# Performance work log

Measured on AMD Instinct MI355X. Metric: run time of the kernel, lower is better.

## Reference

```python
import jax, jax.numpy as jnp
import numpy as np

EPS = 1e-5
CHUNK = 512


def _bn(x, gamma, beta):
    # BatchNorm1d in training mode: biased batch statistics over the batch dim
    m = x.mean(axis=0)
    v = ((x - m) ** 2).mean(axis=0)
    return (x - m) * jax.lax.rsqrt(v + EPS) * gamma + beta


def _xavier(k, fan_in, fan_out):
    lim = float(np.sqrt(6.0 / (fan_in + fan_out)))
    return jax.random.uniform(k, (fan_in, fan_out), minval=-lim, maxval=lim, dtype=jnp.float32)


def setup_inputs() -> dict:
    key = jax.random.key(0)
    ks = jax.random.split(key, 10)
    B, CH_S, CH_H, T = 8192, 512, 2048, 3
    D = CH_H * T  # 6144 = 12 chunks of 512
    inp = {
        "fs": jax.random.normal(ks[0], (B, CH_S), dtype=jnp.float32),
        "ft0": jax.random.normal(ks[1], (B, CH_H), dtype=jnp.float32),
        "ft1": jax.random.normal(ks[2], (B, CH_H), dtype=jnp.float32),
        "ft2": jax.random.normal(ks[3], (B, CH_H), dtype=jnp.float32),
        # fixed (non-trainable in the original: plain tensor) score key [512, 1]
        "score_key": jax.random.uniform(ks[4], (CHUNK, 1), dtype=jnp.float32),
        # align_t: Linear(D,2048) -> BN -> Linear(2048,2048) -> BN -> Linear(2048,CH_H) -> ReLU
        "W1": _xavier(ks[5], D, 2048), "b1": jnp.zeros((2048,), jnp.float32),
        "g1": jnp.ones((2048,), jnp.float32), "beta1": jnp.zeros((2048,), jnp.float32),
        "W2": _xavier(ks[6], 2048, 2048), "b2": jnp.zeros((2048,), jnp.float32),
        "g2": jnp.ones((2048,), jnp.float32), "beta2": jnp.zeros((2048,), jnp.float32),
        "W3": _xavier(ks[7], 2048, CH_H), "b3": jnp.zeros((CH_H,), jnp.float32),
        # extend: Linear(CH_H, D) -> ReLU
        "We": _xavier(ks[8], CH_H, D), "bE": jnp.zeros((D,), jnp.float32),
    }
    return inp


def reference(fs, ft0, ft1, ft2, score_key, W1, b1, g1, beta1, W2, b2, g2, beta2, W3, b3, We, bE):
    # fs is accepted but unused, mirroring the original forward
    ft_all = jnp.concatenate([ft0, ft1, ft2], axis=1)  # [B, D]
    B, D = ft_all.shape
    n_chunks = D // CHUNK
    chunks = ft_all.reshape(B, n_chunks, CHUNK)  # [B, C, 512]
    # chunked score matmul against key[512,1], softmax over chunks
    score = jax.nn.softmax(jnp.einsum("bck,k->bc", chunks, score_key[:, 0]), axis=1)  # [B, C]
    # per-chunk reweighting: x <- x + x*score  == x*(1+score), one broadcasted multiply
    ft_all = (chunks * (1.0 + score[:, :, None])).reshape(B, D)
    # align_t MLP (BatchNorm in training mode, no activation between first layers)
    h = _bn(ft_all @ W1 + b1, g1, beta1)
    h = _bn(h @ W2 + b2, g2, beta2)
    aligned_t = jax.nn.relu(h @ W3 + b3)
    extend_t = jax.nn.relu(aligned_t @ We + bE)
    return aligned_t, extend_t, ft_all
```

## Files before the change

### kernel.cpp

```cpp
#include <hip/hip_runtime.h>
#include <hip/hip_bf16.h>
#include <cstdint>
#include <cstddef>

using bf16x8 = __attribute__((ext_vector_type(8))) __bf16;
using f32x4  = __attribute__((ext_vector_type(4))) float;

__device__ __forceinline__ unsigned short f2bf(float f) {
  unsigned int u = __float_as_uint(f);
  u += 0x7FFFu + ((u >> 16) & 1u);
  return (unsigned short)(u >> 16);
}

__device__ __forceinline__ void async_cp16(const void* g, void* l) {
  __builtin_amdgcn_global_load_lds(
      (const __attribute__((address_space(1))) unsigned int*)g,
      (__attribute__((address_space(3))) unsigned int*)l, 16, 0, 0);
}

__global__ __launch_bounds__(256) void wconv(const float* __restrict__ W,
                                             unsigned short* __restrict__ Wt,
                                             int K, int N) {
  __shared__ float tile[32][33];
  const int n0 = blockIdx.x * 32;
  const int k0 = blockIdx.y * 32;
  const int tx = threadIdx.x;
  const int ty = threadIdx.y;
  for (int i = 0; i < 32; i += 8)
    tile[ty + i][tx] = W[(size_t)(k0 + ty + i) * N + n0 + tx];
  __syncthreads();
  for (int i = 0; i < 32; i += 8)
    Wt[(size_t)(n0 + ty + i) * K + k0 + tx] = f2bf(tile[tx][ty + i]);
}

__global__ __launch_bounds__(256) void score_kernel(
    const float* __restrict__ ft0, const float* __restrict__ ft1,
    const float* __restrict__ ft2, const float* __restrict__ key,
    float* __restrict__ out_f, unsigned short* __restrict__ out_b) {
  const int row  = blockIdx.x;
  const int t    = threadIdx.x;
  const int lane = t & 63;
  const int w    = t >> 6;
  const int h    = t >> 7;
  __shared__ float wsum[6][4];
  __shared__ float mult[12];

  const float4* k4 = (const float4*)key;
  float4 v[6];
#pragma unroll
  for (int i = 0; i < 6; i++) {
    const int idx4 = t + 256 * i;
    const int e    = idx4 * 4;
    const float* tsrc = (i < 2) ? ft0 : (i < 4) ? ft1 : ft2;
    v[i] = *(const float4*)(tsrc + (size_t)row * 2048 + (e & 2047));
    float4 kv = k4[idx4 & 127];
    float p = v[i].x * kv.x + v[i].y * kv.y + v[i].z * kv.z + v[i].w * kv.w;
#pragma unroll
    for (int o = 32; o > 0; o >>= 1) p += __shfl_down(p, o, 64);
    if (lane == 0) wsum[i][w] = p;
  }
  __syncthreads();
  if (t == 0) {
    float s[12];
    float mx = -1e30f;
    for (int c = 0; c < 12; c++) {
      s[c] = wsum[c >> 1][2 * (c & 1)] + wsum[c >> 1][2 * (c & 1) + 1];
      mx = fmaxf(mx, s[c]);
    }
    float tot = 0.f;
    for (int c = 0; c < 12; c++) { s[c] = expf(s[c] - mx); tot += s[c]; }
    const float inv = 1.0f / tot;
    for (int c = 0; c < 12; c++) mult[c] = 1.0f + s[c] * inv;
  }
  __syncthreads();
#pragma unroll
  for (int i = 0; i < 6; i++) {
    const int idx4 = t + 256 * i;
    const int e    = idx4 * 4;
    const float m  = mult[2 * i + h];
    float4 o;
    o.x = v[i].x * m; o.y = v[i].y * m; o.z = v[i].z * m; o.w = v[i].w * m;
    *(float4*)(out_f + (size_t)row * 6144 + e) = o;
    ushort4 ob;
    ob.x = f2bf(o.x); ob.y = f2bf(o.y); ob.z = f2bf(o.z); ob.w = f2bf(o.w);
    *(ushort4*)(out_b + (size_t)row * 6144 + e) = ob;
  }
}

template <int EPI>
__global__ __launch_bounds__(512, 2) void gemm256(
    const unsigned short* __restrict__ A,
    const unsigned short* __restrict__ Bt,
    const float* __restrict__ bias,
    float* __restrict__ C,
    unsigned short* __restrict__ Cbf,
    float* __restrict__ ps,
    float* __restrict__ pq,
    int M, int N, int K) {
  __shared__ __align__(16) unsigned short smem[65536];
  __shared__ float bnred[8][4][16][2];
  const int t    = threadIdx.x;
  const int lane = t & 63;
  const int w    = t >> 6;
  const int wm   = w >> 2;
  const int wn   = w & 3;
  const int frow = lane & 15;
  const int quad = lane >> 4;

  const int NXg  = gridDim.x, NYg = gridDim.y;
  const int blin = blockIdx.x + NXg * blockIdx.y;
  const int rxcd = blin & 7;
  const int ib   = blin >> 3;
  const int RX   = NXg >> 1;
  const int RY   = NYg >> 2;
  const int bx   = (rxcd & 1) * RX + ib % RX;
  const int by   = (rxcd >> 1) * RY + ib / RX;
  const size_t m0 = (size_t)by * 256;
  const size_t n0 = (size_t)bx * 256;

  const bool isB  = w >= 4;
  const int  seg  = (w & 3) * 4096;
  const int  off0 = seg + lane * 16;
  const int  pos0 = off0 ^ (((off0 >> 7) & 7) << 4);
  const int  r0   = pos0 >> 6;
  const int  kb0  = pos0 & 63;
  const unsigned short* gp =
      (isB ? Bt + (n0 + (size_t)r0) * K : A + (m0 + (size_t)r0) * K) + (kb0 >> 1);
  char* lseg = (char*)smem + (isB ? 16384 : 0) + seg;

  const int offA = (wm * 128 + frow) * 64 + quad * 16;
  const int aoff = offA ^ (((offA >> 7) & 7) << 4);
  const int offB = (wn * 64 + frow) * 64 + quad * 16;
  const int boff = 16384 + (offB ^ (((offB >> 7) & 7) << 4));

  f32x4 acc[8][4];
  const f32x4 z = {0.f, 0.f, 0.f, 0.f};
#pragma unroll
  for (int i = 0; i < 8; i++)
#pragma unroll
    for (int j = 0; j < 4; j++) acc[i][j] = z;

  const int nkt = K >> 5;

  auto stage = [&](int slot) {
    char* lb = lseg + slot * 32768;
    async_cp16(gp,                  lb);
    async_cp16(gp + (size_t)16 * K, lb + 1024);
    async_cp16(gp + (size_t)32 * K, lb + 2048);
    async_cp16(gp + (size_t)48 * K, lb + 3072);
    gp += 32;
  };

  auto ldfrag = [&](int slot, bf16x8* fa, bf16x8* fb) {
    const char* base = (const char*)smem + slot * 32768;
#pragma unroll
    for (int mi = 0; mi < 8; ++mi)
      fa[mi] = *(const bf16x8*)(base + aoff + mi * 1024);
#pragma unroll
    for (int ni = 0; ni < 4; ++ni)
      fb[ni] = *(const bf16x8*)(base + boff + ni * 1024);
  };

  auto domfma = [&](const bf16x8* fa, const bf16x8* fb) {
    __builtin_amdgcn_s_setprio(1);
#pragma unroll
    for (int mi = 0; mi < 8; ++mi)
#pragma unroll
      for (int ni = 0; ni < 4; ++ni)
        acc[mi][ni] = __builtin_amdgcn_mfma_f32_16x16x32_bf16(fa[mi], fb[ni], acc[mi][ni], 0, 0, 0);
    __builtin_amdgcn_s_setprio(0);
  };

  bf16x8 fa0[8], fb0[4], fa1[8], fb1[4];

  stage(0); stage(1); stage(2);
  asm volatile("s_waitcnt vmcnt(4)\n\ts_barrier" ::: "memory");
  ldfrag(0, fa0, fb0);

  int kt = 0;
  for (; kt + 4 < nkt; kt += 2) {
    stage((kt + 3) & 3);
    domfma(fa0, fb0);
    ldfrag((kt + 1) & 3, fa1, fb1);
    asm volatile("s_waitcnt vmcnt(4)\n\ts_barrier" ::: "memory");
    stage((kt + 4) & 3);
    domfma(fa1, fb1);
    ldfrag((kt + 2) & 3, fa0, fb0);
    asm volatile("s_waitcnt vmcnt(4)\n\ts_barrier" ::: "memory");
  }
  stage((nkt - 1) & 3);
  domfma(fa0, fb0);
  ldfrag((nkt - 3) & 3, fa1, fb1);
  asm volatile("s_waitcnt vmcnt(4)\n\ts_barrier" ::: "memory");
  domfma(fa1, fb1);
  ldfrag((nkt - 2) & 3, fa0, fb0);
  asm volatile("s_waitcnt vmcnt(0)\n\ts_barrier" ::: "memory");
  domfma(fa0, fb0);
  ldfrag((nkt - 1) & 3, fa1, fb1);
  domfma(fa1, fb1);

  float s4[4] = {0.f, 0.f, 0.f, 0.f};
  float q4[4] = {0.f, 0.f, 0.f, 0.f};
#pragma unroll
  for (int mi = 0; mi < 8; ++mi) {
    const size_t rowb = m0 + wm * 128 + mi * 16 + quad * 4;
#pragma unroll
    for (int ni = 0; ni < 4; ++ni) {
      const size_t col = n0 + wn * 64 + ni * 16 + frow;
      const float bvs = bias[col];
#pragma unroll
      for (int r = 0; r < 4; ++r) {
        float v = acc[mi][ni][r] + bvs;
        if (EPI == 1) v = fmaxf(v, 0.f);
        const size_t idx = (rowb + r) * (size_t)N + col;
        C[idx] = v;
        if (EPI == 1 && Cbf != nullptr) Cbf[idx] = f2bf(v);
        if (EPI == 0) { s4[ni] += v; q4[ni] += v * v; }
      }
    }
  }
  if (EPI == 0) {
#pragma unroll
    for (int ni = 0; ni < 4; ++ni) {
      s4[ni] += __shfl_down(s4[ni], 16, 64);
      s4[ni] += __shfl_down(s4[ni], 32, 64);
      q4[ni] += __shfl_down(q4[ni], 16, 64);
      q4[ni] += __shfl_down(q4[ni], 32, 64);
    }
    if (quad == 0) {
#pragma unroll
      for (int ni = 0; ni < 4; ++ni) {
        bnred[w][ni][frow][0] = s4[ni];
        bnred[w][ni][frow][1] = q4[ni];
      }
    }
    __syncthreads();
    if (w < 4 && quad == 0) {
#pragma unroll
      for (int ni = 0; ni < 4; ++ni) {
        const size_t col = n0 + (size_t)w * 64 + ni * 16 + frow;
        const float ss = bnred[w][ni][frow][0] + bnred[w + 4][ni][frow][0];
        const float qq = bnred[w][ni][frow][1] + bnred[w + 4][ni][frow][1];
        ps[(size_t)by * N + col] = ss;
        pq[(size_t)by * N + col] = qq;
      }
    }
  }
}

__global__ __launch_bounds__(256) void bn_final(const float* __restrict__ ps,
                                                const float* __restrict__ pq,
                                                const float* __restrict__ g,
                                                const float* __restrict__ beta,
                                                float* __restrict__ stats,
                                                int N, int nb, float invM) {
  const int c = blockIdx.x * 256 + threadIdx.x;
  float s = 0.f, q = 0.f;
  for (int b = 0; b < nb; b++) { s += ps[(size_t)b * N + c]; q += pq[(size_t)b * N + c]; }
  const float mean = s * invM;
  const float var  = q * invM - mean * mean;
  const float sc   = g[c] * rsqrtf(var + 1e-5f);
  stats[c]     = sc;
  stats[N + c] = beta[c] - mean * sc;
}

__global__ __launch_bounds__(256) void bn_norm(const float* __restrict__ h,
                                               const float* __restrict__ stats,
                                               unsigned short* __restrict__ hb, int N) {
  const size_t i4 = (size_t)blockIdx.x * 256 + threadIdx.x;
  const float4 x = ((const float4*)h)[i4];
  const int c = (int)((i4 * 4) & (size_t)(N - 1));
  const float4 sc = *(const float4*)(stats + c);
  const float4 tt = *(const float4*)(stats + N + c);
  ushort4 ob;
  ob.x = f2bf(x.x * sc.x + tt.x);
  ob.y = f2bf(x.y * sc.y + tt.y);
  ob.z = f2bf(x.z * sc.z + tt.z);
  ob.w = f2bf(x.w * sc.w + tt.w);
  ((ushort4*)hb)[i4] = ob;
}

extern "C" void kernel_launch(void* const* d_in, const int* in_sizes, int n_in,
                              void* d_out, int out_size, void* d_ws, size_t ws_size,
                              hipStream_t stream) {
  const float* ft0 = (const float*)d_in[1];
  const float* ft1 = (const float*)d_in[2];
  const float* ft2 = (const float*)d_in[3];
  const float* key = (const float*)d_in[4];
  const float* W1  = (const float*)d_in[5];
  const float* b1  = (const float*)d_in[6];
  const float* g1  = (const float*)d_in[7];
  const float* be1 = (const float*)d_in[8];
  const float* W2  = (const float*)d_in[9];
  const float* b2  = (const float*)d_in[10];
  const float* g2  = (const float*)d_in[11];
  const float* be2 = (const float*)d_in[12];
  const float* W3  = (const float*)d_in[13];
  const float* b3  = (const float*)d_in[14];
  const float* We  = (const float*)d_in[15];
  const float* bE  = (const float*)d_in[16];

  float* out         = (float*)d_out;
  float* out_aligned = out;
  float* out_extend  = out + (size_t)8192 * 2048;
  float* out_ft      = out + (size_t)8192 * 2048 + (size_t)8192 * 6144;

  char* ws = (char*)d_ws;
  unsigned short* ft_bf = (unsigned short*)(ws);
  unsigned short* Wt1   = (unsigned short*)(ws + 100663296ull);
  unsigned short* Wt2   = (unsigned short*)(ws + 125829120ull);
  unsigned short* Wt3   = (unsigned short*)(ws + 134217728ull);
  unsigned short* WtE   = (unsigned short*)(ws + 142606336ull);
  float*          hf    = (float*)(ws + 167772160ull);
  unsigned short* hba   = (unsigned short*)(ws + 234881024ull);
  unsigned short* hbb   = (unsigned short*)(ws + 268435456ull);
  float*          psum  = (float*)(ws + 301989888ull);
  float*          psq   = (float*)(ws + 302252032ull);
  float*          stats = (float*)(ws + 302514176ull);

  const dim3 blk32(32, 8);
  wconv<<<dim3(2048 / 32, 6144 / 32), blk32, 0, stream>>>(W1, Wt1, 6144, 2048);
  wconv<<<dim3(2048 / 32, 2048 / 32), blk32, 0, stream>>>(W2, Wt2, 2048, 2048);
  wconv<<<dim3(2048 / 32, 2048 / 32), blk32, 0, stream>>>(W3, Wt3, 2048, 2048);
  wconv<<<dim3(6144 / 32, 2048 / 32), blk32, 0, stream>>>(We, WtE, 2048, 6144);

  score_kernel<<<dim3(8192), dim3(256), 0, stream>>>(ft0, ft1, ft2, key, out_ft, ft_bf);

  gemm256<0><<<dim3(8, 32), dim3(512), 0, stream>>>(ft_bf, Wt1, b1, hf,
                                                    (unsigned short*)nullptr, psum, psq,
                                                    8192, 2048, 6144);
  bn_final<<<dim3(8), dim3(256), 0, stream>>>(psum, psq, g1, be1, stats, 2048, 32, 1.0f / 8192.0f);
  bn_norm<<<dim3(16384), dim3(256), 0, stream>>>(hf, stats, hba, 2048);

  gemm256<0><<<dim3(8, 32), dim3(512), 0, stream>>>(hba, Wt2, b2, hf,
                                                    (unsigned short*)nullptr, psum, psq,
                                                    8192, 2048, 2048);
  bn_final<<<dim3(8), dim3(256), 0, stream>>>(psum, psq, g2, be2, stats, 2048, 32, 1.0f / 8192.0f);
  bn_norm<<<dim3(16384), dim3(256), 0, stream>>>(hf, stats, hba, 2048);

  gemm256<1><<<dim3(8, 32), dim3(512), 0, stream>>>(hba, Wt3, b3, out_aligned, hbb,
                                                    (float*)nullptr, (float*)nullptr,
                                                    8192, 2048, 2048);
  gemm256<1><<<dim3(24, 32), dim3(512), 0, stream>>>(hbb, WtE, bE, out_extend,
                                                     (unsigned short*)nullptr,
                                                     (float*)nullptr, (float*)nullptr,
                                                     8192, 6144, 2048);
}
```

Before: 1.345 ms.

## Fold BatchNorm into next layer weights and switch GEMM to 32x32 MFMA

The BatchNorm scale and shift are folded into the following linear layer. Its weights are scaled per input row during the bf16 transpose, and the shift is turned into an adjusted bias through a small matrix-vector product. This removes the separate fp32 hidden write and the bn_norm pass: GEMMs now write pre-BN activations in bf16 directly. The GEMM also moves from 16x16x32 to 32x32x16 MFMA tiles and drops the XCD-aware block remapping. In exchange, BN statistics are computed from values later rounded to bf16, and the weight scaling adds rounding error when variances are small.

```diff
diff --git a/kernel.cpp b/kernel.cpp
--- a/kernel.cpp
+++ b/kernel.cpp
@@ -5,6 +5,7 @@
 
 using bf16x8 = __attribute__((ext_vector_type(8))) __bf16;
 using f32x4  = __attribute__((ext_vector_type(4))) float;
+using f32x16 = __attribute__((ext_vector_type(16))) float;
 
 __device__ __forceinline__ unsigned short f2bf(float f) {
   unsigned int u = __float_as_uint(f);
@@ -33,6 +34,41 @@
     Wt[(size_t)(n0 + ty + i) * K + k0 + tx] = f2bf(tile[tx][ty + i]);
 }
 
+__global__ __launch_bounds__(256) void wscale_t(const float* __restrict__ W,
+                                                const float* __restrict__ sc,
+                                                unsigned short* __restrict__ Wt,
+                                                int K, int N) {
+  __shared__ float tile[32][33];
+  const int n0 = blockIdx.x * 32;
+  const int k0 = blockIdx.y * 32;
+  const int tx = threadIdx.x;
+  const int ty = threadIdx.y;
+  for (int i = 0; i < 32; i += 8)
+    tile[ty + i][tx] = W[(size_t)(k0 + ty + i) * N + n0 + tx] * sc[k0 + ty + i];
+  __syncthreads();
+  for (int i = 0; i < 32; i += 8)
+    Wt[(size_t)(n0 + ty + i) * K + k0 + tx] = f2bf(tile[tx][ty + i]);
+}
+
+__global__ __launch_bounds__(256) void bvec_p(const float* __restrict__ W,
+                                              const float* __restrict__ tt,
+                                              float* __restrict__ pb, int N) {
+  const int c  = blockIdx.x * 256 + threadIdx.x;
+  const int k0 = blockIdx.y * 256;
+  float s = 0.f;
+  for (int k = 0; k < 256; ++k) s += tt[k0 + k] * W[(size_t)(k0 + k) * N + c];
+  pb[(size_t)blockIdx.y * N + c] = s;
+}
+
+__global__ __launch_bounds__(256) void bvec_f(const float* __restrict__ pb,
+                                              const float* __restrict__ b,
+                                              float* __restrict__ bs, int N, int nb) {
+  const int c = blockIdx.x * 256 + threadIdx.x;
+  float s = b[c];
+  for (int j = 0; j < nb; ++j) s += pb[(size_t)j * N + c];
+  bs[c] = s;
+}
+
 __global__ __launch_bounds__(256) void score_kernel(
     const float* __restrict__ ft0, const float* __restrict__ ft1,
     const float* __restrict__ ft2, const float* __restrict__ key,
@@ -98,23 +134,14 @@
     float* __restrict__ pq,
     int M, int N, int K) {
   __shared__ __align__(16) unsigned short smem[65536];
-  __shared__ float bnred[8][4][16][2];
+  __shared__ float bnred[8][2][32][2];
   const int t    = threadIdx.x;
   const int lane = t & 63;
   const int w    = t >> 6;
   const int wm   = w >> 2;
   const int wn   = w & 3;
-  const int frow = lane & 15;
-  const int quad = lane >> 4;
-
-  const int NXg  = gridDim.x, NYg = gridDim.y;
-  const int blin = blockIdx.x + NXg * blockIdx.y;
-  const int rxcd = blin & 7;
-  const int ib   = blin >> 3;
-  const int RX   = NXg >> 1;
-  const int RY   = NYg >> 2;
-  const int bx   = (rxcd & 1) * RX + ib % RX;
-  const int by   = (rxcd >> 1) * RY + ib / RX;
+  const int bx   = blockIdx.x;
+  const int by   = blockIdx.y;
   const size_t m0 = (size_t)by * 256;
   const size_t n0 = (size_t)bx * 256;
 
@@ -128,17 +155,19 @@
       (isB ? Bt + (n0 + (size_t)r0) * K : A + (m0 + (size_t)r0) * K) + (kb0 >> 1);
   char* lseg = (char*)smem + (isB ? 16384 : 0) + seg;
 
-  const int offA = (wm * 128 + frow) * 64 + quad * 16;
-  const int aoff = offA ^ (((offA >> 7) & 7) << 4);
-  const int offB = (wn * 64 + frow) * 64 + quad * 16;
-  const int boff = 16384 + (offB ^ (((offB >> 7) & 7) << 4));
-
-  f32x4 acc[8][4];
-  const f32x4 z = {0.f, 0.f, 0.f, 0.f};
-#pragma unroll
-  for (int i = 0; i < 8; i++)
-#pragma unroll
-    for (int j = 0; j < 4; j++) acc[i][j] = z;
+  const int r5  = lane & 31;
+  const int q16 = lane >> 5;
+  const int swz = ((r5 >> 1) & 7) << 4;
+  const int aBase = (((wm * 128 + r5) * 64 + q16 * 16) ^ swz);
+  const int bBase = 16384 + (((wn * 64 + r5) * 64 + q16 * 16) ^ swz);
+
+  f32x16 acc[4][2];
+#pragma unroll
+  for (int i = 0; i < 4; i++)
+#pragma unroll
+    for (int j = 0; j < 2; j++)
+#pragma unroll
+      for (int g = 0; g < 16; g++) acc[i][j][g] = 0.f;
 
   const int nkt = K >> 5;
 
@@ -154,20 +183,27 @@
   auto ldfrag = [&](int slot, bf16x8* fa, bf16x8* fb) {
     const char* base = (const char*)smem + slot * 32768;
 #pragma unroll
-    for (int mi = 0; mi < 8; ++mi)
-      fa[mi] = *(const bf16x8*)(base + aoff + mi * 1024);
-#pragma unroll
-    for (int ni = 0; ni < 4; ++ni)
-      fb[ni] = *(const bf16x8*)(base + boff + ni * 1024);
+    for (int mi = 0; mi < 4; ++mi) {
+      fa[mi * 2 + 0] = *(const bf16x8*)(base + (aBase       ) + mi * 2048);
+      fa[mi * 2 + 1] = *(const bf16x8*)(base + (aBase ^ 32  ) + mi * 2048);
+    }
+#pragma unroll
+    for (int ni = 0; ni < 2; ++ni) {
+      fb[ni * 2 + 0] = *(const bf16x8*)(base + (bBase       ) + ni * 2048);
+      fb[ni * 2 + 1] = *(const bf16x8*)(base + (bBase ^ 32  ) + ni * 2048);
+    }
   };
 
   auto domfma = [&](const bf16x8* fa, const bf16x8* fb) {
     __builtin_amdgcn_s_setprio(1);
 #pragma unroll
-    for (int mi = 0; mi < 8; ++mi)
-#pragma unroll
-      for (int ni = 0; ni < 4; ++ni)
-        acc[mi][ni] = __builtin_amdgcn_mfma_f32_16x16x32_bf16(fa[mi], fb[ni], acc[mi][ni], 0, 0, 0);
+    for (int kh = 0; kh < 2; ++kh)
+#pragma unroll
+      for (int mi = 0; mi < 4; ++mi)
+#pragma unroll
+        for (int ni = 0; ni < 2; ++ni)
+          acc[mi][ni] = __builtin_amdgcn_mfma_f32_32x32x16_bf16(
+              fa[mi * 2 + kh], fb[ni * 2 + kh], acc[mi][ni], 0, 0, 0);
     __builtin_amdgcn_s_setprio(0);
   };
 
@@ -199,50 +235,62 @@
   ldfrag((nkt - 1) & 3, fa1, fb1);
   domfma(fa1, fb1);
 
-  float s4[4] = {0.f, 0.f, 0.f, 0.f};
-  float q4[4] = {0.f, 0.f, 0.f, 0.f};
-#pragma unroll
-  for (int mi = 0; mi < 8; ++mi) {
-    const size_t rowb = m0 + wm * 128 + mi * 16 + quad * 4;
-#pragma unroll
-    for (int ni = 0; ni < 4; ++ni) {
-      const size_t col = n0 + wn * 64 + ni * 16 + frow;
+  const int cl = r5;
+  const int rh = q16 * 4;
+  if (EPI == 0) {
+    float s2[2] = {0.f, 0.f}, q2[2] = {0.f, 0.f};
+#pragma unroll
+    for (int ni = 0; ni < 2; ++ni) {
+      const size_t col = n0 + wn * 64 + ni * 32 + cl;
       const float bvs = bias[col];
 #pragma unroll
-      for (int r = 0; r < 4; ++r) {
-        float v = acc[mi][ni][r] + bvs;
-        if (EPI == 1) v = fmaxf(v, 0.f);
-        const size_t idx = (rowb + r) * (size_t)N + col;
-        C[idx] = v;
-        if (EPI == 1 && Cbf != nullptr) Cbf[idx] = f2bf(v);
-        if (EPI == 0) { s4[ni] += v; q4[ni] += v * v; }
+      for (int mi = 0; mi < 4; ++mi) {
+        const size_t rowb = m0 + wm * 128 + mi * 32 + rh;
+#pragma unroll
+        for (int g = 0; g < 16; ++g) {
+          float v = acc[mi][ni][g] + bvs;
+          const size_t row = rowb + (g & 3) + 8 * (g >> 2);
+          Cbf[row * (size_t)N + col] = f2bf(v);
+          s2[ni] += v; q2[ni] += v * v;
+        }
       }
     }
-  }
-  if (EPI == 0) {
-#pragma unroll
-    for (int ni = 0; ni < 4; ++ni) {
-      s4[ni] += __shfl_down(s4[ni], 16, 64);
-      s4[ni] += __shfl_down(s4[ni], 32, 64);
-      q4[ni] += __shfl_down(q4[ni], 16, 64);
-      q4[ni] += __shfl_down(q4[ni], 32, 64);
-    }
-    if (quad == 0) {
-#pragma unroll
-      for (int ni = 0; ni < 4; ++ni) {
-        bnred[w][ni][frow][0] = s4[ni];
-        bnred[w][ni][frow][1] = q4[ni];
+#pragma unroll
+    for (int ni = 0; ni < 2; ++ni) {
+      s2[ni] += __shfl_down(s2[ni], 32, 64);
+      q2[ni] += __shfl_down(q2[ni], 32, 64);
+    }
+    if (lane < 32) {
+#pragma unroll
+      for (int ni = 0; ni < 2; ++ni) {
+        bnred[w][ni][cl][0] = s2[ni];
+        bnred[w][ni][cl][1] = q2[ni];
       }
     }
     __syncthreads();
-    if (w < 4 && quad == 0) {
-#pragma unroll
-      for (int ni = 0; ni < 4; ++ni) {
-        const size_t col = n0 + (size_t)w * 64 + ni * 16 + frow;
-        const float ss = bnred[w][ni][frow][0] + bnred[w + 4][ni][frow][0];
-        const float qq = bnred[w][ni][frow][1] + bnred[w + 4][ni][frow][1];
-        ps[(size_t)by * N + col] = ss;
-        pq[(size_t)by * N + col] = qq;
+    if (w < 4 && lane < 32) {
+#pragma unroll
+      for (int ni = 0; ni < 2; ++ni) {
+        const size_t col = n0 + (size_t)w * 64 + ni * 32 + cl;
+        ps[(size_t)by * N + col] = bnred[w][ni][cl][0] + bnred[w + 4][ni][cl][0];
+        pq[(size_t)by * N + col] = bnred[w][ni][cl][1] + bnred[w + 4][ni][cl][1];
+      }
+    }
+  } else {
+#pragma unroll
+    for (int ni = 0; ni < 2; ++ni) {
+      const size_t col = n0 + wn * 64 + ni * 32 + cl;
+      const float bvs = bias[col];
+#pragma unroll
+      for (int mi = 0; mi < 4; ++mi) {
+        const size_t rowb = m0 + wm * 128 + mi * 32 + rh;
+#pragma unroll
+        for (int g = 0; g < 16; ++g) {
+          float v = fmaxf(acc[mi][ni][g] + bvs, 0.f);
+          const size_t idx = (rowb + (g & 3) + 8 * (g >> 2)) * (size_t)N + col;
+          C[idx] = v;
+          if (Cbf != nullptr) Cbf[idx] = f2bf(v);
+        }
       }
     }
   }
@@ -262,22 +310,6 @@
   const float sc   = g[c] * rsqrtf(var + 1e-5f);
   stats[c]     = sc;
   stats[N + c] = beta[c] - mean * sc;
-}
-
-__global__ __launch_bounds__(256) void bn_norm(const float* __restrict__ h,
-                                               const float* __restrict__ stats,
-                                               unsigned short* __restrict__ hb, int N) {
-  const size_t i4 = (size_t)blockIdx.x * 256 + threadIdx.x;
-  const float4 x = ((const float4*)h)[i4];
-  const int c = (int)((i4 * 4) & (size_t)(N - 1));
-  const float4 sc = *(const float4*)(stats + c);
-  const float4 tt = *(const float4*)(stats + N + c);
-  ushort4 ob;
-  ob.x = f2bf(x.x * sc.x + tt.x);
-  ob.y = f2bf(x.y * sc.y + tt.y);
-  ob.z = f2bf(x.z * sc.z + tt.z);
-  ob.w = f2bf(x.w * sc.w + tt.w);
-  ((ushort4*)hb)[i4] = ob;
 }
 
 extern "C" void kernel_launch(void* const* d_in, const int* in_sizes, int n_in,
@@ -311,7 +343,9 @@
   unsigned short* Wt2   = (unsigned short*)(ws + 125829120ull);
   unsigned short* Wt3   = (unsigned short*)(ws + 134217728ull);
   unsigned short* WtE   = (unsigned short*)(ws + 142606336ull);
-  float*          hf    = (float*)(ws + 167772160ull);
+  float*          pb    = (float*)(ws + 167772160ull);
+  float*          bsc2  = (float*)(ws + 167837696ull);
+  float*          bsc3  = (float*)(ws + 167845888ull);
   unsigned short* hba   = (unsigned short*)(ws + 234881024ull);
   unsigned short* hbb   = (unsigned short*)(ws + 268435456ull);
   float*          psum  = (float*)(ws + 301989888ull);
@@ -320,28 +354,28 @@
 
   const dim3 blk32(32, 8);
   wconv<<<dim3(2048 / 32, 6144 / 32), blk32, 0, stream>>>(W1, Wt1, 6144, 2048);
-  wconv<<<dim3(2048 / 32, 2048 / 32), blk32, 0, stream>>>(W2, Wt2, 2048, 2048);
-  wconv<<<dim3(2048 / 32, 2048 / 32), blk32, 0, stream>>>(W3, Wt3, 2048, 2048);
   wconv<<<dim3(6144 / 32, 2048 / 32), blk32, 0, stream>>>(We, WtE, 2048, 6144);
 
   score_kernel<<<dim3(8192), dim3(256), 0, stream>>>(ft0, ft1, ft2, key, out_ft, ft_bf);
 
-  gemm256<0><<<dim3(8, 32), dim3(512), 0, stream>>>(ft_bf, Wt1, b1, hf,
-                                                    (unsigned short*)nullptr, psum, psq,
-                                                    8192, 2048, 6144);
+  gemm256<0><<<dim3(8, 32), dim3(512), 0, stream>>>(ft_bf, Wt1, b1, (float*)nullptr, hba,
+                                                    psum, psq, 8192, 2048, 6144);
   bn_final<<<dim3(8), dim3(256), 0, stream>>>(psum, psq, g1, be1, stats, 2048, 32, 1.0f / 8192.0f);
-  bn_norm<<<dim3(16384), dim3(256), 0, stream>>>(hf, stats, hba, 2048);
-
-  gemm256<0><<<dim3(8, 32), dim3(512), 0, stream>>>(hba, Wt2, b2, hf,
-                                                    (unsigned short*)nullptr, psum, psq,
-                                                    8192, 2048, 2048);
+  wscale_t<<<dim3(64, 64), blk32, 0, stream>>>(W2, stats, Wt2, 2048, 2048);
+  bvec_p<<<dim3(8, 8), dim3(256), 0, stream>>>(W2, stats + 2048, pb, 2048);
+  bvec_f<<<dim3(8), dim3(256), 0, stream>>>(pb, b2, bsc2, 2048, 8);
+
+  gemm256<0><<<dim3(8, 32), dim3(512), 0, stream>>>(hba, Wt2, bsc2, (float*)nullptr, hbb,
+                                                    psum, psq, 8192, 2048, 2048);
   bn_final<<<dim3(8), dim3(256), 0, stream>>>(psum, psq, g2, be2, stats, 2048, 32, 1.0f / 8192.0f);
-  bn_norm<<<dim3(16384), dim3(256), 0, stream>>>(hf, stats, hba, 2048);
-
-  gemm256<1><<<dim3(8, 32), dim3(512), 0, stream>>>(hba, Wt3, b3, out_aligned, hbb,
+  wscale_t<<<dim3(64, 64), blk32, 0, stream>>>(W3, stats, Wt3, 2048, 2048);
+  bvec_p<<<dim3(8, 8), dim3(256), 0, stream>>>(W3, stats + 2048, pb, 2048);
+  bvec_f<<<dim3(8), dim3(256), 0, stream>>>(pb, b3, bsc3, 2048, 8);
+
+  gemm256<1><<<dim3(8, 32), dim3(512), 0, stream>>>(hbb, Wt3, bsc3, out_aligned, hba,
                                                     (float*)nullptr, (float*)nullptr,
                                                     8192, 2048, 2048);
-  gemm256<1><<<dim3(24, 32), dim3(512), 0, stream>>>(hbb, WtE, bE, out_extend,
+  gemm256<1><<<dim3(24, 32), dim3(512), 0, stream>>>(hba, WtE, bE, out_extend,
                                                      (unsigned short*)nullptr,
                                                      (float*)nullptr, (float*)nullptr,
                                                      8192, 6144, 2048);
```

New measurement: 1.358 ms. Within noise of the previous version (+0.9%).
